# Kernel tuning notes

Measured on AMD Instinct MI355X. Metric: run time of the kernel, lower is better.

The kernel has to match this reference:

```python
import jax, jax.numpy as jnp
import numpy as np

N = 2048      # atoms in one graph
C = 8         # energy_num_channels
CONV = 332.07156


def setup_inputs() -> dict:
    key = jax.random.key(0)
    ks = jax.random.split(key, 12)
    X = jax.random.normal(ks[0], (N, 3), dtype=jnp.float32) * 10.0   # coords (Angstrom-ish)
    embs = jax.random.normal(ks[1], (N, C), dtype=jnp.float32)        # GNN atom embeddings
    qs = jax.random.normal(ks[2], (N,), dtype=jnp.float32) * 0.5      # partial charges
    Ps = jnp.zeros((N, 3), dtype=jnp.float32)                          # dipoles (zeros, as in EnergyNet.forward)
    w0 = jax.random.uniform(ks[3], (N,), dtype=jnp.float32) * 0.5 + 0.1  # vdw_dep
    s0 = jax.random.uniform(ks[4], (N,), dtype=jnp.float32) + 1.0        # vdw_sig
    chainidx = jax.random.randint(ks[5], (N,), 0, 2)
    sf_elec = jax.random.normal(ks[6], (2 * C + 1, 1), dtype=jnp.float32) * 0.1
    sf_elec = sf_elec.at[-1, 0].set(1.0)
    born_factor = jax.random.normal(ks[7], (C,), dtype=jnp.float32) * 0.1 + 1.0
    die_factor = jax.random.normal(ks[8], (C,), dtype=jnp.float32) * 0.1 + 4.0
    depth_factor = jax.random.normal(ks[9], (2 * C, 1), dtype=jnp.float32) * 0.05 + 1.0
    radius_factor = jax.random.normal(ks[10], (2 * C, 1), dtype=jnp.float32) * 0.05 + 1.0
    return dict(X=X, embs=embs, qs=qs, Ps=Ps, w0=w0, s0=s0, chainidx=chainidx,
                sf_elec=sf_elec, born_factor=born_factor, die_factor=die_factor,
                depth_factor=depth_factor, radius_factor=radius_factor)


def _nan_guard(e):
    return jnp.where(jnp.isnan(e), jnp.asarray(1e-6, e.dtype), e)


def _energies(X, embs, qs, Ps, w0, s0, mask, sf_elec, born, die, depth, radius):
    # shared pairwise geometry (original recomputes this in each submodule)
    V = X[None, :, :] - X[:, None, :]               # V[i,j] = X[j]-X[i], [N,N,3]
    D = jnp.sqrt(jnp.sum(V * V + 1e-6, axis=-1))    # [N,N]
    Vp = V + 1e-6
    Vn = Vp / jnp.maximum(jnp.linalg.norm(Vp, axis=-1, keepdims=True), 1e-12)
    invD = 1.0 / (D + 1e-6)

    # ---- Electrostatics ----
    f = sf_elec[:, 0]
    # screening = emb_j . f[:C] + emb_i . f[C:2C] + invD * f[2C]  (decomposed matmul)
    sf = (embs @ f[:C])[None, :] + (embs @ f[C:2 * C])[:, None] + invD * f[2 * C]
    OqP = jnp.einsum('ijk,ik->ij', Vn, Ps)
    OPP = Ps @ Ps.T
    Q12 = jnp.outer(qs, qs)
    invD3 = invD * invD * invD
    E_qq = Q12 * invD * sf
    E_qP = OqP * invD * invD3
    E_PP = OPP * invD3 * invD3
    E_elec = 0.5 * jnp.sum(CONV * mask * (E_qq + E_qP + E_PP))
    E_elec = _nan_guard(E_elec)

    # ---- Solvation (calc_pair=False => only Born self term) ----
    atomic_die = embs @ die + 1e-6
    R = embs @ born + 1.0
    E_self = -(1.0 - 1.0 / atomic_die) * qs / (R + 1e-6)
    E_solv = CONV * jnp.sum(E_self) * 0.01
    E_solv = _nan_guard(E_solv)

    # ---- vdW ----
    rf = radius[:, 0]
    df = depth[:, 0]
    sig_r = jax.nn.sigmoid((embs @ rf[:C])[None, :] + (embs @ rf[C:])[:, None])
    # NB: original broadcasting makes s0_ij = 2*s0[j] (column-only), reproduced faithfully
    s = (2.0 * s0)[None, :] * (0.8 * sig_r + 0.4)
    repl = 5.0 * jnp.exp(-0.3 * D * D * D) * mask
    Dm = D - s
    attr = (jnp.exp(-(Dm - 0.3) ** 2) + jnp.exp(-3.0 * Dm * Dm)
            + jnp.exp(-10.0 * Dm * Dm)) / 3.0 * mask
    w0j = jnp.sqrt(w0 * w0 + 1e-6)[None, :]        # original w0_ij also column-only
    sig_d = jax.nn.sigmoid((embs @ df[:C])[None, :] + (embs @ df[C:])[:, None])
    w = w0j * (sig_d + 0.5)
    E_vdw = jnp.sum(-w * attr + repl)
    E_vdw = _nan_guard(E_vdw)

    return E_vdw, E_elec, E_solv


def reference(X, embs, qs, Ps, w0, s0, chainidx, sf_elec, born_factor, die_factor,
              depth_factor, radius_factor):
    mask = (chainidx[None, :] != chainidx[:, None]).astype(X.dtype)
    return _energies(X, embs, qs, Ps, w0, s0, mask,
                     sf_elec, born_factor, die_factor, depth_factor, radius_factor)
```

## Files before the change

kernel.cpp:

```cpp
#include <hip/hip_runtime.h>

#define NA 2048
#define CDIM 8
#define CONVF 332.07156f
#define TI 4
#define PAIR_GRID 516


__global__ __launch_bounds__(256) void precompute_kernel(
    const float* __restrict__ X,
    const float* __restrict__ embs,
    const float* __restrict__ qs,
    const float* __restrict__ Ps,
    const float* __restrict__ w0,
    const float* __restrict__ s0,
    const int* __restrict__ chain,
    const float* __restrict__ sf_elec,
    const float* __restrict__ born,
    const float* __restrict__ die,
    const float* __restrict__ depth,
    const float* __restrict__ radius,
    int* __restrict__ cnt,
    float4* __restrict__ u0, float4* __restrict__ u1,
    float4* __restrict__ u2, float4* __restrict__ u3,
    float* __restrict__ d_out)
{
    int i = blockIdx.x * 256 + threadIdx.x;
    float e_self = 0.0f;
    int c0 = 0;
    {
        float e[CDIM];
#pragma unroll
        for (int k = 0; k < CDIM; ++k) e[k] = embs[i * CDIM + k];
        float sfA = 0.f, sfB = 0.f, rfA = 0.f, rfB = 0.f, dfA = 0.f, dfB = 0.f;
        float dieV = 0.f, Rv = 0.f;
#pragma unroll
        for (int k = 0; k < CDIM; ++k) {
            sfA  += e[k] * sf_elec[k];
            sfB  += e[k] * sf_elec[CDIM + k];
            rfA  += e[k] * radius[k];
            rfB  += e[k] * radius[CDIM + k];
            dfA  += e[k] * depth[k];
            dfB  += e[k] * depth[CDIM + k];
            dieV += e[k] * die[k];
            Rv   += e[k] * born[k];
        }
        dieV += 1e-6f;
        Rv += 1.0f;
        float q = qs[i];
        e_self = -(1.0f - 1.0f / dieV) * q / (Rv + 1e-6f);

        float erA = __expf(-rfA), edA = __expf(-dfA);
        float erB = __expf(-rfB), edB = __expf(-dfB);
        float w0j = sqrtf(w0[i] * w0[i] + 1e-6f);

        u0[i] = make_float4(X[i * 3 + 0], X[i * 3 + 1], X[i * 3 + 2], q);
        u1[i] = make_float4(sfA, erA, edA, w0j);
        u2[i] = make_float4(2.0f * s0[i], Ps[i * 3 + 0], Ps[i * 3 + 1], Ps[i * 3 + 2]);
        u3[i] = make_float4(sfB, erB, edB, 0.0f);
        c0 = (chain[i] == 0) ? 1 : 0;
    }
#pragma unroll
    for (int off = 32; off > 0; off >>= 1) {
        e_self += __shfl_down(e_self, off);
        c0     += __shfl_down(c0, off);
    }
    __shared__ float ss[4];
    __shared__ int sc[4];
    int lane = threadIdx.x & 63, wid = threadIdx.x >> 6;
    if (lane == 0) { ss[wid] = e_self; sc[wid] = c0; }
    __syncthreads();
    if (threadIdx.x == 0) {
        atomicAdd(d_out + 2, CONVF * 0.01f * (ss[0] + ss[1] + ss[2] + ss[3]));
        atomicAdd(cnt + 0, sc[0] + sc[1] + sc[2] + sc[3]);
    }
}

__global__ __launch_bounds__(256) void scatter_kernel(
    const int* __restrict__ chain, int* __restrict__ cnt,
    const float4* __restrict__ u0, const float4* __restrict__ u1,
    const float4* __restrict__ u2, const float4* __restrict__ u3,
    float4* __restrict__ g0, float4* __restrict__ g1,
    float4* __restrict__ g2, float4* __restrict__ g3)
{
    int i = blockIdx.x * 256 + threadIdx.x;
    int n0 = cnt[0];
    int slot = (chain[i] == 0) ? atomicAdd(cnt + 1, 1)
                               : n0 + atomicAdd(cnt + 2, 1);
    g0[slot] = u0[i];
    g1[slot] = u1[i];
    g2[slot] = u2[i];
    g3[slot] = u3[i];
}

__global__ __launch_bounds__(256) void pair_kernel(
    const int* __restrict__ cnt,
    const float4* __restrict__ g0, const float4* __restrict__ g1,
    const float4* __restrict__ g2, const float4* __restrict__ g3,
    const float* __restrict__ sf_elec,
    float* __restrict__ d_out)
{
    const int b = blockIdx.x, tid = threadIdx.x;
    const int n0 = cnt[0];
    const int B0 = (n0 + TI - 1) / TI;
    const int n1 = NA - n0;
    const int B1 = (n1 + TI - 1) / TI;
    if (b >= B0 + B1) return;

    int rbase, rend, jbeg, jend;
    if (b < B0) { rbase = b * TI;             rend = n0; jbeg = n0; jend = NA; }
    else        { rbase = n0 + (b - B0) * TI; rend = NA; jbeg = 0;  jend = n0; }

    const float f16 = sf_elec[2 * CDIM];

    float xi[TI], yi[TI], zi[TI], qi[TI], sfB[TI], erB[TI], edB[TI], val[TI];
    float psx[TI], psy[TI], psz[TI];
    bool hasPs = false;
#pragma unroll
    for (int t = 0; t < TI; ++t) {
        int r = rbase + t;
        val[t] = (r < rend) ? 1.0f : 0.0f;
        r = min(r, rend - 1);
        float4 p0 = g0[r], p3 = g3[r], p2 = g2[r];
        xi[t] = p0.x; yi[t] = p0.y; zi[t] = p0.z; qi[t] = p0.w;
        sfB[t] = p3.x; erB[t] = p3.y; edB[t] = p3.z;
        psx[t] = p2.y; psy[t] = p2.z; psz[t] = p2.w;
        hasPs = hasPs || (psx[t] != 0.0f) || (psy[t] != 0.0f) || (psz[t] != 0.0f);
    }

    float acc_e[TI], acc_v[TI];
#pragma unroll
    for (int t = 0; t < TI; ++t) { acc_e[t] = 0.f; acc_v[t] = 0.f; }

    const float* g2f = (const float*)g2;

#pragma unroll 2
    for (int j = jbeg + tid; j < jend; j += 256) {
        const float4 a = g0[j];
        const float4 bb = g1[j];
        float s0x2, pjx = 0.f, pjy = 0.f, pjz = 0.f;
        if (hasPs) {
            float4 c2 = g2[j];
            s0x2 = c2.x; pjx = c2.y; pjy = c2.z; pjz = c2.w;
        } else {
            s0x2 = g2f[4 * j];
        }

#pragma unroll
        for (int t = 0; t < TI; ++t) {
            const float dx = a.x - xi[t], dy = a.y - yi[t], dz = a.z - zi[t];
            const float d2 = dx * dx + dy * dy + dz * dz + 3e-6f;
            const float D = sqrtf(d2);
            const float invD = __builtin_amdgcn_rcpf(D + 1e-6f);

            const float sf = bb.x + sfB[t] + invD * f16;
            float ee = qi[t] * a.w * invD * sf;
            if (hasPs) {
                const float vpx = dx + 1e-6f, vpy = dy + 1e-6f, vpz = dz + 1e-6f;
                float vn = sqrtf(vpx * vpx + vpy * vpy + vpz * vpz);
                vn = fmaxf(vn, 1e-12f);
                const float OqP = (vpx * psx[t] + vpy * psy[t] + vpz * psz[t]) *
                                  __builtin_amdgcn_rcpf(vn);
                const float OPP = psx[t] * pjx + psy[t] * pjy + psz[t] * pjz;
                const float invD2 = invD * invD;
                const float invD4 = invD2 * invD2;
                const float invD6 = invD4 * invD2;
                ee += OqP * invD4 + OPP * invD6;
            }
            acc_e[t] += ee;

            const float sig_r = __builtin_amdgcn_rcpf(fmaf(bb.y, erB[t], 1.0f));
            const float s = s0x2 * fmaf(0.8f, sig_r, 0.4f);
            const float Dm = D - s;
            const float Dm2 = Dm * Dm;
            const float t1 = __expf(-Dm2);
            const float ta = t1 * __expf(fmaf(0.6f, Dm, -0.09f));
            const float t2 = t1 * t1;
            const float t3 = t2 * t1;
            const float t4 = t2 * t2;
            const float t8 = t4 * t4;
            const float t10 = t8 * t2;
            const float attr = ta + t3 + t10;
            const float sig_d = __builtin_amdgcn_rcpf(fmaf(bb.z, edB[t], 1.0f));
            const float w = bb.w * (sig_d + 0.5f);
            const float repl = 5.0f * __expf(-0.3f * D * d2);
            acc_v[t] += repl - w * attr * (1.0f / 3.0f);
        }
    }

    float ae = 0.f, av = 0.f;
#pragma unroll
    for (int t = 0; t < TI; ++t) {
        ae += val[t] * acc_e[t];
        av += val[t] * acc_v[t];
    }
#pragma unroll
    for (int off = 32; off > 0; off >>= 1) {
        ae += __shfl_down(ae, off);
        av += __shfl_down(av, off);
    }
    __shared__ float se[4], sv[4];
    int lane = tid & 63, wid = tid >> 6;
    if (lane == 0) { se[wid] = ae; sv[wid] = av; }
    __syncthreads();
    if (tid == 0) {
        atomicAdd(d_out + 1, 0.5f * CONVF * (se[0] + se[1] + se[2] + se[3]));
        atomicAdd(d_out + 0, sv[0] + sv[1] + sv[2] + sv[3]);
    }
}

extern "C" void kernel_launch(void* const* d_in, const int* in_sizes, int n_in,
                              void* d_out, int out_size, void* d_ws, size_t ws_size,
                              hipStream_t stream) {
    const float* X       = (const float*)d_in[0];
    const float* embs    = (const float*)d_in[1];
    const float* qs      = (const float*)d_in[2];
    const float* Ps      = (const float*)d_in[3];
    const float* w0      = (const float*)d_in[4];
    const float* s0      = (const float*)d_in[5];
    const int*   chain   = (const int*)d_in[6];
    const float* sf_elec = (const float*)d_in[7];
    const float* born    = (const float*)d_in[8];
    const float* die     = (const float*)d_in[9];
    const float* depth   = (const float*)d_in[10];
    const float* radius  = (const float*)d_in[11];
    float* out = (float*)d_out;

    int* cnt = (int*)d_ws;
    float4* u0 = (float4*)((char*)d_ws + 16);
    float4* u1 = u0 + NA;
    float4* u2 = u1 + NA;
    float4* u3 = u2 + NA;
    float4* g0 = u3 + NA;
    float4* g1 = g0 + NA;
    float4* g2 = g1 + NA;
    float4* g3 = g2 + NA;

    hipMemsetAsync(d_out, 0, 3 * sizeof(float), stream);
    hipMemsetAsync(d_ws, 0, 16, stream);
    precompute_kernel<<<NA / 256, 256, 0, stream>>>(
        X, embs, qs, Ps, w0, s0, chain, sf_elec, born, die, depth, radius,
        cnt, u0, u1, u2, u3, out);
    scatter_kernel<<<NA / 256, 256, 0, stream>>>(chain, cnt, u0, u1, u2, u3,
                                                 g0, g1, g2, g3);
    pair_kernel<<<PAIR_GRID, 256, 0, stream>>>(cnt, g0, g1, g2, g3, sf_elec, out);
}
```

Measured before the change: 102.1 us.

## Fuse precompute and chain partition into one single-block kernel with prefix scan

```diff
diff --git a/kernel.cpp b/kernel.cpp
--- a/kernel.cpp
+++ b/kernel.cpp
@@ -7,7 +7,7 @@
 #define PAIR_GRID 516
 
 
-__global__ __launch_bounds__(256) void precompute_kernel(
+__global__ __launch_bounds__(1024) void pre_kernel(
     const float* __restrict__ X,
     const float* __restrict__ embs,
     const float* __restrict__ qs,
@@ -20,15 +20,21 @@
     const float* __restrict__ die,
     const float* __restrict__ depth,
     const float* __restrict__ radius,
-    int* __restrict__ cnt,
-    float4* __restrict__ u0, float4* __restrict__ u1,
-    float4* __restrict__ u2, float4* __restrict__ u3,
+    int* __restrict__ wsi,
+    float4* __restrict__ g0, float4* __restrict__ g1,
+    float4* __restrict__ g2, float4* __restrict__ g3,
     float* __restrict__ d_out)
 {
-    int i = blockIdx.x * 256 + threadIdx.x;
-    float e_self = 0.0f;
-    int c0 = 0;
-    {
+    const int t = threadIdx.x;
+    const int i0 = 2 * t, i1 = 2 * t + 1;
+
+    float4 a0[2], a1[2], a2[2], a3[2];
+    int flag[2];
+    float es = 0.0f;
+
+#pragma unroll
+    for (int h = 0; h < 2; ++h) {
+        const int i = (h == 0) ? i0 : i1;
         float e[CDIM];
 #pragma unroll
         for (int k = 0; k < CDIM; ++k) e[k] = embs[i * CDIM + k];
@@ -47,50 +53,65 @@
         }
         dieV += 1e-6f;
         Rv += 1.0f;
-        float q = qs[i];
-        e_self = -(1.0f - 1.0f / dieV) * q / (Rv + 1e-6f);
-
-        float erA = __expf(-rfA), edA = __expf(-dfA);
-        float erB = __expf(-rfB), edB = __expf(-dfB);
-        float w0j = sqrtf(w0[i] * w0[i] + 1e-6f);
-
-        u0[i] = make_float4(X[i * 3 + 0], X[i * 3 + 1], X[i * 3 + 2], q);
-        u1[i] = make_float4(sfA, erA, edA, w0j);
-        u2[i] = make_float4(2.0f * s0[i], Ps[i * 3 + 0], Ps[i * 3 + 1], Ps[i * 3 + 2]);
-        u3[i] = make_float4(sfB, erB, edB, 0.0f);
-        c0 = (chain[i] == 0) ? 1 : 0;
-    }
-#pragma unroll
-    for (int off = 32; off > 0; off >>= 1) {
-        e_self += __shfl_down(e_self, off);
-        c0     += __shfl_down(c0, off);
-    }
-    __shared__ float ss[4];
-    __shared__ int sc[4];
-    int lane = threadIdx.x & 63, wid = threadIdx.x >> 6;
-    if (lane == 0) { ss[wid] = e_self; sc[wid] = c0; }
+        const float q = qs[i];
+        es += -(1.0f - 1.0f / dieV) * q / (Rv + 1e-6f);
+
+        const float erB = __expf(-rfB), edB = __expf(-dfB);
+        const float erA = __expf(-rfA), edA = __expf(-dfA);
+        const float w0j = sqrtf(w0[i] * w0[i] + 1e-6f);
+
+        a0[h] = make_float4(X[i * 3 + 0], X[i * 3 + 1], X[i * 3 + 2], q);
+        a1[h] = make_float4(sfA, erA, edA, w0j);
+        a2[h] = make_float4(2.0f * s0[i], Ps[i * 3 + 0], Ps[i * 3 + 1], Ps[i * 3 + 2]);
+        a3[h] = make_float4(sfB, erB, edB, 0.0f);
+        flag[h] = (chain[i] == 0) ? 1 : 0;
+    }
+
+    const int lane = t & 63, wv = t >> 6;
+    int cnt = flag[0] + flag[1];
+    int x = cnt;
+#pragma unroll
+    for (int off = 1; off < 64; off <<= 1) {
+        int y = __shfl_up(x, off);
+        if (lane >= off) x += y;
+    }
+    const int excl = x - cnt;
+
+    __shared__ int wsum[16];
+    __shared__ float fsum[16];
+    if (lane == 63) wsum[wv] = x;
+    float esw = es;
+#pragma unroll
+    for (int off = 32; off > 0; off >>= 1) esw += __shfl_down(esw, off);
+    if (lane == 0) fsum[wv] = esw;
     __syncthreads();
-    if (threadIdx.x == 0) {
-        atomicAdd(d_out + 2, CONVF * 0.01f * (ss[0] + ss[1] + ss[2] + ss[3]));
-        atomicAdd(cnt + 0, sc[0] + sc[1] + sc[2] + sc[3]);
-    }
-}
-
-__global__ __launch_bounds__(256) void scatter_kernel(
-    const int* __restrict__ chain, int* __restrict__ cnt,
-    const float4* __restrict__ u0, const float4* __restrict__ u1,
-    const float4* __restrict__ u2, const float4* __restrict__ u3,
-    float4* __restrict__ g0, float4* __restrict__ g1,
-    float4* __restrict__ g2, float4* __restrict__ g3)
-{
-    int i = blockIdx.x * 256 + threadIdx.x;
-    int n0 = cnt[0];
-    int slot = (chain[i] == 0) ? atomicAdd(cnt + 1, 1)
-                               : n0 + atomicAdd(cnt + 2, 1);
-    g0[slot] = u0[i];
-    g1[slot] = u1[i];
-    g2[slot] = u2[i];
-    g3[slot] = u3[i];
+
+    int wbase = 0, tot = 0;
+#pragma unroll
+    for (int k = 0; k < 16; ++k) {
+        int v = wsum[k];
+        if (k < wv) wbase += v;
+        tot += v;
+    }
+    const int base = wbase + excl;
+
+    const int p0_0 = base;
+    const int slot0 = flag[0] ? p0_0 : tot + (i0 - p0_0);
+    const int p0_1 = base + flag[0];
+    const int slot1 = flag[1] ? p0_1 : tot + (i1 - p0_1);
+
+    g0[slot0] = a0[0]; g1[slot0] = a1[0]; g2[slot0] = a2[0]; g3[slot0] = a3[0];
+    g0[slot1] = a0[1]; g1[slot1] = a1[1]; g2[slot1] = a2[1]; g3[slot1] = a3[1];
+
+    if (t == 0) {
+        float tt = 0.f;
+#pragma unroll
+        for (int k = 0; k < 16; ++k) tt += fsum[k];
+        d_out[2] = CONVF * 0.01f * tt;
+        d_out[0] = 0.0f;
+        d_out[1] = 0.0f;
+        wsi[0] = tot;
+    }
 }
 
 __global__ __launch_bounds__(256) void pair_kernel(
@@ -121,6 +142,7 @@
         int r = rbase + t;
         val[t] = (r < rend) ? 1.0f : 0.0f;
         r = min(r, rend - 1);
+        r = max(r, 0);
         float4 p0 = g0[r], p3 = g3[r], p2 = g2[r];
         xi[t] = p0.x; yi[t] = p0.y; zi[t] = p0.z; qi[t] = p0.w;
         sfB[t] = p3.x; erB[t] = p3.y; edB[t] = p3.z;
@@ -200,7 +222,7 @@
         av += __shfl_down(av, off);
     }
     __shared__ float se[4], sv[4];
-    int lane = tid & 63, wid = tid >> 6;
+    const int lane = tid & 63, wid = tid >> 6;
     if (lane == 0) { se[wid] = ae; sv[wid] = av; }
     __syncthreads();
     if (tid == 0) {
@@ -226,22 +248,14 @@
     const float* radius  = (const float*)d_in[11];
     float* out = (float*)d_out;
 
-    int* cnt = (int*)d_ws;
-    float4* u0 = (float4*)((char*)d_ws + 16);
-    float4* u1 = u0 + NA;
-    float4* u2 = u1 + NA;
-    float4* u3 = u2 + NA;
-    float4* g0 = u3 + NA;
+    int* wsi = (int*)d_ws;
+    float4* g0 = (float4*)((char*)d_ws + 128);
     float4* g1 = g0 + NA;
     float4* g2 = g1 + NA;
     float4* g3 = g2 + NA;
 
-    hipMemsetAsync(d_out, 0, 3 * sizeof(float), stream);
-    hipMemsetAsync(d_ws, 0, 16, stream);
-    precompute_kernel<<<NA / 256, 256, 0, stream>>>(
+    pre_kernel<<<1, 1024, 0, stream>>>(
         X, embs, qs, Ps, w0, s0, chain, sf_elec, born, die, depth, radius,
-        cnt, u0, u1, u2, u3, out);
-    scatter_kernel<<<NA / 256, 256, 0, stream>>>(chain, cnt, u0, u1, u2, u3,
-                                                 g0, g1, g2, g3);
-    pair_kernel<<<PAIR_GRID, 256, 0, stream>>>(cnt, g0, g1, g2, g3, sf_elec, out);
+        wsi, g0, g1, g2, g3, out);
+    pair_kernel<<<PAIR_GRID, 256, 0, stream>>>(wsi, g0, g1, g2, g3, sf_elec, out);
 }
```

Measured after the change: 97.52 us. 1.05x faster.
